# Performance work log

Hardware: AMD Instinct MI355X
Metric: run time of the kernel (lower is better)

## Reference

```python
import jax, jax.numpy as jnp
import numpy as np

E, D, H, T = 8, 1024, 4096, 32768  # experts, model dim, ffn hidden dim, total tokens


def setup_inputs() -> dict:
    key = jax.random.key(0)
    kx, k1, k2, k3 = jax.random.split(key, 4)
    x = jax.random.normal(kx, (T, D), dtype=jnp.float32)
    w1 = jax.random.normal(k1, (E, D, H), dtype=jnp.float32)
    w2 = jax.random.normal(k2, (E, H, D), dtype=jnp.float32)
    w3 = jax.random.normal(k3, (E, D, H), dtype=jnp.float32)
    # uniform token-to-expert split, matching the source's splits = [T//E]*E
    splits = jnp.full((E,), T // E, dtype=jnp.int32)
    return {"x": x, "w1": w1, "w2": w2, "w3": w3, "splits": splits}


def reference(x, w1, w2, w3, splits):
    # splits is uniform (T//E per expert), so torch.split + per-expert matmul +
    # concat is exactly a batched (grouped) GEMM over the expert axis.
    E, D, H = w1.shape
    xe = x.reshape(E, -1, D)  # [E, T//E, D]
    gate = jnp.einsum('etd,edh->eth', xe, w1)  # w1 projection
    up = jnp.einsum('etd,edh->eth', xe, w3)    # w3 projection
    h = jax.nn.silu(gate) * up                 # fused SwiGLU activation
    out = jnp.einsum('eth,ehd->etd', h, w2)    # down projection
    return out.reshape(x.shape)
```

## Files before the change

kernel.cpp:

```cpp
#include <hip/hip_runtime.h>
#include <stdint.h>

#define E_  8
#define D_  1024
#define H_  4096
#define T_  32768
#define TPE 4096

typedef __bf16 bf16x8 __attribute__((ext_vector_type(8)));
typedef float  f32x4  __attribute__((ext_vector_type(4)));
typedef unsigned short u16x4 __attribute__((ext_vector_type(4)));
typedef unsigned short u16x8 __attribute__((ext_vector_type(8)));

__device__ __forceinline__ unsigned short f2bf(float f) {
  union { float f; uint32_t u; } v; v.f = f;
  uint32_t u = v.u;
  return (unsigned short)((u + 0x7FFFu + ((u >> 16) & 1u)) >> 16);
}

__device__ __forceinline__ void gld16(const unsigned short* g, unsigned short* l) {
  __builtin_amdgcn_global_load_lds(
      (const __attribute__((address_space(1))) unsigned int*)g,
      (__attribute__((address_space(3))) unsigned int*)l, 16, 0, 0);
}

__device__ __forceinline__ f32x4 mfma_bf16(bf16x8 a, bf16x8 b, f32x4 c) {
  return __builtin_amdgcn_mfma_f32_16x16x32_bf16(a, b, c, 0, 0, 0);
}

__global__ void cvt_bf16(const float* __restrict__ in, unsigned short* __restrict__ out) {
  size_t i = ((size_t)blockIdx.x * 256 + threadIdx.x) * 8;
  float4 a = *(const float4*)(in + i);
  float4 b = *(const float4*)(in + i + 4);
  u16x8 o;
  o[0] = f2bf(a.x); o[1] = f2bf(a.y); o[2] = f2bf(a.z); o[3] = f2bf(a.w);
  o[4] = f2bf(b.x); o[5] = f2bf(b.y); o[6] = f2bf(b.z); o[7] = f2bf(b.w);
  *(u16x8*)(out + i) = o;
}

__global__ void transpose_bf16(const float* __restrict__ in, unsigned short* __restrict__ out,
                               int R, int C) {
  __shared__ unsigned short t[64][68];
  size_t eo = (size_t)blockIdx.z * R * C;
  const float* ine = in + eo;
  unsigned short* oute = out + eo;
  int r0 = blockIdx.y * 64, c0 = blockIdx.x * 64;
  int rl = threadIdx.x >> 4;
  int cl = (threadIdx.x & 15) * 4;
#pragma unroll
  for (int i = 0; i < 4; ++i) {
    int r = i * 16 + rl;
    float4 v = *(const float4*)(ine + (size_t)(r0 + r) * C + c0 + cl);
    t[cl + 0][r] = f2bf(v.x);
    t[cl + 1][r] = f2bf(v.y);
    t[cl + 2][r] = f2bf(v.z);
    t[cl + 3][r] = f2bf(v.w);
  }
  __syncthreads();
#pragma unroll
  for (int i = 0; i < 4; ++i) {
    int c = i * 16 + rl;
    *(u16x4*)(oute + (size_t)(c0 + c) * R + r0 + cl) = *(const u16x4*)&t[c][cl];
  }
}

__global__ void transpose_ilv_bf16(const float* __restrict__ in, unsigned short* __restrict__ out,
                                   int R, int C, int off) {
  __shared__ unsigned short t[64][68];
  const float* ine = in + (size_t)blockIdx.z * R * C;
  unsigned short* oute = out + (size_t)blockIdx.z * 2 * (size_t)R * C;
  int r0 = blockIdx.y * 64, c0 = blockIdx.x * 64;
  int rl = threadIdx.x >> 4;
  int cl = (threadIdx.x & 15) * 4;
#pragma unroll
  for (int i = 0; i < 4; ++i) {
    int r = i * 16 + rl;
    float4 v = *(const float4*)(ine + (size_t)(r0 + r) * C + c0 + cl);
    t[cl + 0][r] = f2bf(v.x);
    t[cl + 1][r] = f2bf(v.y);
    t[cl + 2][r] = f2bf(v.z);
    t[cl + 3][r] = f2bf(v.w);
  }
  __syncthreads();
#pragma unroll
  for (int i = 0; i < 4; ++i) {
    int c = i * 16 + rl;
    int rr = c0 + c;
    int orow = 32 * (rr >> 4) + (rr & 15) + off;
    *(u16x4*)(oute + (size_t)orow * R + r0 + cl) = *(const u16x4*)&t[c][cl];
  }
}

template<int KT>
__device__ __forceinline__ void gemm_core(
    const unsigned short* __restrict__ A,
    const unsigned short* __restrict__ B,
    const int K, const int m0, const int n0,
    unsigned short* sm, f32x4 (&acc)[8][4]) {
  const int tid  = threadIdx.x;
  const int w    = tid >> 6;
  const int lane = tid & 63;
  const int wr = w >> 2, wc = w & 3;
  const int lr = lane & 15, lk = lane >> 4;

  const unsigned short* gA[4];
  const unsigned short* gB[4];
#pragma unroll
  for (int q = 0; q < 4; ++q) {
    const int rg = 4 * q + (w >> 1);
    const size_t ro = (size_t)(rg * 16 + lr) * K + (w & 1) * 32 + lk * 8;
    gA[q] = A + (size_t)m0 * K + ro;
    gB[q] = B + (size_t)n0 * K + ro;
  }

#pragma unroll
  for (int q = 0; q < 4; ++q) gld16(gA[q], sm + (w + 8 * q) * 512);
#pragma unroll
  for (int q = 0; q < 4; ++q) gld16(gB[q], sm + 32768 + (w + 8 * q) * 512);
  gld16(gB[0] + 64, sm + 32768 + 16384 + (w + 0) * 512);
  gld16(gB[1] + 64, sm + 32768 + 16384 + (w + 8) * 512);
  gld16(gA[0] + 64, sm + 16384 + (w + 0) * 512);
  gld16(gA[1] + 64, sm + 16384 + (w + 8) * 512);
  asm volatile("s_waitcnt vmcnt(4)" ::: "memory");
  __builtin_amdgcn_s_barrier();

  bf16x8 a[4][2], bb[4][2];

#pragma unroll 1
  for (int u = 0; u < KT; ++u) {
    const int bu = u & 1;
    unsigned short* cA = sm + bu * 16384;
    unsigned short* cB = sm + 32768 + bu * 16384;
    unsigned short* nA = sm + (bu ^ 1) * 16384;
    unsigned short* nB = sm + 32768 + (bu ^ 1) * 16384;
    const int koff1 = (u + 1) * 64, koff2 = (u + 2) * 64;

#pragma unroll
    for (int i = 0; i < 4; ++i)
#pragma unroll
      for (int kc = 0; kc < 2; ++kc)
        a[i][kc] = *(const bf16x8*)(cA + ((wr * 8 + i) * 2 + kc) * 512 + lane * 8);
#pragma unroll
    for (int j = 0; j < 2; ++j)
#pragma unroll
      for (int kc = 0; kc < 2; ++kc)
        bb[j][kc] = *(const bf16x8*)(cB + ((wc * 4 + j) * 2 + kc) * 512 + lane * 8);
    if (u + 1 < KT) {
      gld16(gA[2] + koff1, nA + (w + 16) * 512);
      gld16(gA[3] + koff1, nA + (w + 24) * 512);
    }
    __builtin_amdgcn_s_barrier();
    asm volatile("s_waitcnt lgkmcnt(0)" ::: "memory");
    __builtin_amdgcn_sched_barrier(0);
    __builtin_amdgcn_s_setprio(1);
#pragma unroll
    for (int i = 0; i < 4; ++i)
#pragma unroll
      for (int j = 0; j < 2; ++j)
#pragma unroll
        for (int kc = 0; kc < 2; ++kc)
          acc[i][j] = mfma_bf16(a[i][kc], bb[j][kc], acc[i][j]);
    __builtin_amdgcn_s_setprio(0);
    __builtin_amdgcn_s_barrier();

#pragma unroll
    for (int j = 0; j < 2; ++j)
#pragma unroll
      for (int kc = 0; kc < 2; ++kc)
        bb[2 + j][kc] = *(const bf16x8*)(cB + ((wc * 4 + 2 + j) * 2 + kc) * 512 + lane * 8);
    if (u + 1 < KT) {
      gld16(gB[2] + koff1, nB + (w + 16) * 512);
      gld16(gB[3] + koff1, nB + (w + 24) * 512);
    }
    __builtin_amdgcn_s_barrier();
    asm volatile("s_waitcnt lgkmcnt(0)" ::: "memory");
    __builtin_amdgcn_sched_barrier(0);
    __builtin_amdgcn_s_setprio(1);
#pragma unroll
    for (int i = 0; i < 4; ++i)
#pragma unroll
      for (int j = 0; j < 2; ++j)
#pragma unroll
        for (int kc = 0; kc < 2; ++kc)
          acc[i][2 + j] = mfma_bf16(a[i][kc], bb[2 + j][kc], acc[i][2 + j]);
    __builtin_amdgcn_s_setprio(0);
    __builtin_amdgcn_s_barrier();

#pragma unroll
    for (int i = 0; i < 4; ++i)
#pragma unroll
      for (int kc = 0; kc < 2; ++kc)
        a[i][kc] = *(const bf16x8*)(cA + ((wr * 8 + 4 + i) * 2 + kc) * 512 + lane * 8);
    if (u + 2 < KT) {
      gld16(gB[0] + koff2, cB + (w + 0) * 512);
      gld16(gB[1] + koff2, cB + (w + 8) * 512);
    }
    __builtin_amdgcn_s_barrier();
    asm volatile("s_waitcnt lgkmcnt(0)" ::: "memory");
    __builtin_amdgcn_sched_barrier(0);
    __builtin_amdgcn_s_setprio(1);
#pragma unroll
    for (int i = 0; i < 4; ++i)
#pragma unroll
      for (int j = 0; j < 2; ++j)
#pragma unroll
        for (int kc = 0; kc < 2; ++kc)
          acc[4 + i][j] = mfma_bf16(a[i][kc], bb[j][kc], acc[4 + i][j]);
    __builtin_amdgcn_s_setprio(0);
    __builtin_amdgcn_s_barrier();

    if (u + 2 < KT) {
      gld16(gA[0] + koff2, cA + (w + 0) * 512);
      gld16(gA[1] + koff2, cA + (w + 8) * 512);
    }
    __builtin_amdgcn_s_barrier();
    __builtin_amdgcn_s_setprio(1);
#pragma unroll
    for (int i = 0; i < 4; ++i)
#pragma unroll
      for (int j = 0; j < 2; ++j)
#pragma unroll
        for (int kc = 0; kc < 2; ++kc)
          acc[4 + i][2 + j] = mfma_bf16(a[i][kc], bb[2 + j][kc], acc[4 + i][2 + j]);
    __builtin_amdgcn_s_setprio(0);
    if (u == KT - 2) {
      asm volatile("s_waitcnt vmcnt(0)" ::: "memory");
    } else {
      asm volatile("s_waitcnt vmcnt(4)" ::: "memory");
    }
    __builtin_amdgcn_s_barrier();
  }
}

__global__ __launch_bounds__(512, 2) void gemm_gateup(
    const unsigned short* __restrict__ xb,
    const unsigned short* __restrict__ w13t,
    unsigned short* __restrict__ hbuf) {
  __shared__ __align__(16) unsigned short sm[65536];
  const int e = blockIdx.z;
  const int bid = blockIdx.x;
  const int sb = (bid & 7) * 64 + (bid >> 3);
  const int mb = sb & 15, nb = sb >> 4;
  const int m0 = mb * 256, n0 = nb * 256;

  f32x4 acc[8][4] = {};
  gemm_core<D_ / 64>(xb + (size_t)e * TPE * D_,
                     w13t + (size_t)e * (2 * H_) * D_,
                     D_, m0, n0, sm, acc);

  const int tid = threadIdx.x;
  const int w = tid >> 6, lane = tid & 63;
  const int wr = w >> 2, wc = w & 3, lr = lane & 15, lk = lane >> 4;
  unsigned short* He = hbuf + (size_t)e * TPE * H_;
  const int rbase = m0 + wr * 128;
  const int cbase = n0 / 2 + wc * 32;
#pragma unroll
  for (int i = 0; i < 8; ++i)
#pragma unroll
    for (int jp = 0; jp < 2; ++jp)
#pragma unroll
      for (int r = 0; r < 4; ++r) {
        float g  = acc[i][2 * jp][r];
        float uu = acc[i][2 * jp + 1][r];
        float hv = (g / (1.0f + __expf(-g))) * uu;
        He[(size_t)(rbase + i * 16 + lk * 4 + r) * H_ + cbase + jp * 16 + lr] = f2bf(hv);
      }
}

__global__ __launch_bounds__(512, 2) void gemm_down(
    const unsigned short* __restrict__ hbuf,
    const unsigned short* __restrict__ w2t,
    float* __restrict__ out) {
  __shared__ __align__(16) unsigned short sm[65536];
  const int e = blockIdx.z;
  const int bid = blockIdx.x;
  const int sb = (bid & 7) * 8 + (bid >> 3);
  const int mb = sb & 15, nb = sb >> 4;
  const int m0 = mb * 256, n0 = nb * 256;

  f32x4 acc[8][4] = {};
  gemm_core<H_ / 64>(hbuf + (size_t)e * TPE * H_,
                     w2t + (size_t)e * (size_t)D_ * H_,
                     H_, m0, n0, sm, acc);

  const int tid = threadIdx.x;
  const int w = tid >> 6, lane = tid & 63;
  const int wr = w >> 2, wc = w & 3, lr = lane & 15, lk = lane >> 4;
  float* Oe = out + (size_t)e * TPE * D_;
  const int rbase = m0 + wr * 128;
  const int cbase = n0 + wc * 64;
#pragma unroll
  for (int i = 0; i < 8; ++i)
#pragma unroll
    for (int j = 0; j < 4; ++j)
#pragma unroll
      for (int r = 0; r < 4; ++r)
        Oe[(size_t)(rbase + i * 16 + lk * 4 + r) * D_ + cbase + j * 16 + lr] = acc[i][j][r];
}

extern "C" void kernel_launch(void* const* d_in, const int* in_sizes, int n_in,
                              void* d_out, int out_size, void* d_ws, size_t ws_size,
                              hipStream_t stream) {
  const float* x  = (const float*)d_in[0];
  const float* w1 = (const float*)d_in[1];
  const float* w2 = (const float*)d_in[2];
  const float* w3 = (const float*)d_in[3];

  char* ws = (char*)d_ws;
  unsigned short* xb   = (unsigned short*)(ws);
  unsigned short* w13t = (unsigned short*)(ws + (64ull << 20));
  unsigned short* w2t  = (unsigned short*)(ws + (192ull << 20));
  unsigned short* hbuf = (unsigned short*)(ws + (256ull << 20));
  float* out = (float*)d_out;

  cvt_bf16<<<(T_ * D_) / 2048, 256, 0, stream>>>(x, xb);
  transpose_ilv_bf16<<<dim3(H_ / 64, D_ / 64, E_), 256, 0, stream>>>(w1, w13t, D_, H_, 0);
  transpose_ilv_bf16<<<dim3(H_ / 64, D_ / 64, E_), 256, 0, stream>>>(w3, w13t, D_, H_, 16);
  transpose_bf16<<<dim3(D_ / 64, H_ / 64, E_), 256, 0, stream>>>(w2, w2t, H_, D_);

  gemm_gateup<<<dim3(512, 1, E_), 512, 0, stream>>>(xb, w13t, hbuf);

  gemm_down<<<dim3(64, 1, E_), 512, 0, stream>>>(hbuf, w2t, out);
}
```

Before: 1.360 ms.

## Switch GEMM core from 16x16x32 to 32x32x16 bf16 MFMA tiles

Replaces the 16x16x32 MFMA instruction with the 32x32x16 variant in the shared GEMM core. This changes the LDS fragment layout, the global-to-LDS load addressing, the w1/w3 interleave granularity (32-row groups) and both epilogues to match the 32x32 accumulator layout. Larger MFMA tiles mean fewer instructions and fewer LDS reads per FLOP. The trade-off is a different register pressure profile and epilogue store pattern.

```diff
diff --git a/kernel.cpp b/kernel.cpp
--- a/kernel.cpp
+++ b/kernel.cpp
@@ -9,6 +9,7 @@
 
 typedef __bf16 bf16x8 __attribute__((ext_vector_type(8)));
 typedef float  f32x4  __attribute__((ext_vector_type(4)));
+typedef float  f32x16 __attribute__((ext_vector_type(16)));
 typedef unsigned short u16x4 __attribute__((ext_vector_type(4)));
 typedef unsigned short u16x8 __attribute__((ext_vector_type(8)));
 
@@ -24,8 +25,8 @@
       (__attribute__((address_space(3))) unsigned int*)l, 16, 0, 0);
 }
 
-__device__ __forceinline__ f32x4 mfma_bf16(bf16x8 a, bf16x8 b, f32x4 c) {
-  return __builtin_amdgcn_mfma_f32_16x16x32_bf16(a, b, c, 0, 0, 0);
+__device__ __forceinline__ f32x16 mfma32(bf16x8 a, bf16x8 b, f32x16 c) {
+  return __builtin_amdgcn_mfma_f32_32x32x16_bf16(a, b, c, 0, 0, 0);
 }
 
 __global__ void cvt_bf16(const float* __restrict__ in, unsigned short* __restrict__ out) {
@@ -86,7 +87,7 @@
   for (int i = 0; i < 4; ++i) {
     int c = i * 16 + rl;
     int rr = c0 + c;
-    int orow = 32 * (rr >> 4) + (rr & 15) + off;
+    int orow = 64 * (rr >> 5) + (rr & 31) + off;
     *(u16x4*)(oute + (size_t)orow * R + r0 + cl) = *(const u16x4*)&t[c][cl];
   }
 }
@@ -96,19 +97,21 @@
     const unsigned short* __restrict__ A,
     const unsigned short* __restrict__ B,
     const int K, const int m0, const int n0,
-    unsigned short* sm, f32x4 (&acc)[8][4]) {
+    unsigned short* sm, f32x16 (&acc)[4][2]) {
   const int tid  = threadIdx.x;
   const int w    = tid >> 6;
   const int lane = tid & 63;
   const int wr = w >> 2, wc = w & 3;
-  const int lr = lane & 15, lk = lane >> 4;
+  const int lr = lane & 31;
+  const int lh = lane >> 5;
 
   const unsigned short* gA[4];
   const unsigned short* gB[4];
 #pragma unroll
   for (int q = 0; q < 4; ++q) {
-    const int rg = 4 * q + (w >> 1);
-    const size_t ro = (size_t)(rg * 16 + lr) * K + (w & 1) * 32 + lk * 8;
+    const int c  = w + 8 * q;
+    const int rb = c >> 2, kc = c & 3;
+    const size_t ro = (size_t)(rb * 32 + lr) * K + kc * 16 + lh * 8;
     gA[q] = A + (size_t)m0 * K + ro;
     gB[q] = B + (size_t)n0 * K + ro;
   }
@@ -124,7 +127,7 @@
   asm volatile("s_waitcnt vmcnt(4)" ::: "memory");
   __builtin_amdgcn_s_barrier();
 
-  bf16x8 a[4][2], bb[4][2];
+  bf16x8 a[2][4], bb[2][4];
 
 #pragma unroll 1
   for (int u = 0; u < KT; ++u) {
@@ -136,15 +139,13 @@
     const int koff1 = (u + 1) * 64, koff2 = (u + 2) * 64;
 
 #pragma unroll
-    for (int i = 0; i < 4; ++i)
-#pragma unroll
-      for (int kc = 0; kc < 2; ++kc)
-        a[i][kc] = *(const bf16x8*)(cA + ((wr * 8 + i) * 2 + kc) * 512 + lane * 8);
-#pragma unroll
-    for (int j = 0; j < 2; ++j)
-#pragma unroll
-      for (int kc = 0; kc < 2; ++kc)
-        bb[j][kc] = *(const bf16x8*)(cB + ((wc * 4 + j) * 2 + kc) * 512 + lane * 8);
+    for (int i = 0; i < 2; ++i)
+#pragma unroll
+      for (int ks = 0; ks < 4; ++ks)
+        a[i][ks] = *(const bf16x8*)(cA + ((wr * 4 + i) * 4 + ks) * 512 + lane * 8);
+#pragma unroll
+    for (int ks = 0; ks < 4; ++ks)
+      bb[0][ks] = *(const bf16x8*)(cB + ((wc * 2 + 0) * 4 + ks) * 512 + lane * 8);
     if (u + 1 < KT) {
       gld16(gA[2] + koff1, nA + (w + 16) * 512);
       gld16(gA[3] + koff1, nA + (w + 24) * 512);
@@ -154,20 +155,16 @@
     __builtin_amdgcn_sched_barrier(0);
     __builtin_amdgcn_s_setprio(1);
 #pragma unroll
-    for (int i = 0; i < 4; ++i)
-#pragma unroll
-      for (int j = 0; j < 2; ++j)
-#pragma unroll
-        for (int kc = 0; kc < 2; ++kc)
-          acc[i][j] = mfma_bf16(a[i][kc], bb[j][kc], acc[i][j]);
+    for (int ks = 0; ks < 4; ++ks)
+#pragma unroll
+      for (int i = 0; i < 2; ++i)
+        acc[i][0] = mfma32(a[i][ks], bb[0][ks], acc[i][0]);
     __builtin_amdgcn_s_setprio(0);
     __builtin_amdgcn_s_barrier();
 
 #pragma unroll
-    for (int j = 0; j < 2; ++j)
-#pragma unroll
-      for (int kc = 0; kc < 2; ++kc)
-        bb[2 + j][kc] = *(const bf16x8*)(cB + ((wc * 4 + 2 + j) * 2 + kc) * 512 + lane * 8);
+    for (int ks = 0; ks < 4; ++ks)
+      bb[1][ks] = *(const bf16x8*)(cB + ((wc * 2 + 1) * 4 + ks) * 512 + lane * 8);
     if (u + 1 < KT) {
       gld16(gB[2] + koff1, nB + (w + 16) * 512);
       gld16(gB[3] + koff1, nB + (w + 24) * 512);
@@ -177,20 +174,18 @@
     __builtin_amdgcn_sched_barrier(0);
     __builtin_amdgcn_s_setprio(1);
 #pragma unroll
-    for (int i = 0; i < 4; ++i)
-#pragma unroll
-      for (int j = 0; j < 2; ++j)
-#pragma unroll
-        for (int kc = 0; kc < 2; ++kc)
-          acc[i][2 + j] = mfma_bf16(a[i][kc], bb[2 + j][kc], acc[i][2 + j]);
+    for (int ks = 0; ks < 4; ++ks)
+#pragma unroll
+      for (int i = 0; i < 2; ++i)
+        acc[i][1] = mfma32(a[i][ks], bb[1][ks], acc[i][1]);
     __builtin_amdgcn_s_setprio(0);
     __builtin_amdgcn_s_barrier();
 
 #pragma unroll
-    for (int i = 0; i < 4; ++i)
-#pragma unroll
-      for (int kc = 0; kc < 2; ++kc)
-        a[i][kc] = *(const bf16x8*)(cA + ((wr * 8 + 4 + i) * 2 + kc) * 512 + lane * 8);
+    for (int i = 0; i < 2; ++i)
+#pragma unroll
+      for (int ks = 0; ks < 4; ++ks)
+        a[i][ks] = *(const bf16x8*)(cA + ((wr * 4 + 2 + i) * 4 + ks) * 512 + lane * 8);
     if (u + 2 < KT) {
       gld16(gB[0] + koff2, cB + (w + 0) * 512);
       gld16(gB[1] + koff2, cB + (w + 8) * 512);
@@ -200,12 +195,10 @@
     __builtin_amdgcn_sched_barrier(0);
     __builtin_amdgcn_s_setprio(1);
 #pragma unroll
-    for (int i = 0; i < 4; ++i)
-#pragma unroll
-      for (int j = 0; j < 2; ++j)
-#pragma unroll
-        for (int kc = 0; kc < 2; ++kc)
-          acc[4 + i][j] = mfma_bf16(a[i][kc], bb[j][kc], acc[4 + i][j]);
+    for (int ks = 0; ks < 4; ++ks)
+#pragma unroll
+      for (int i = 0; i < 2; ++i)
+        acc[2 + i][0] = mfma32(a[i][ks], bb[0][ks], acc[2 + i][0]);
     __builtin_amdgcn_s_setprio(0);
     __builtin_amdgcn_s_barrier();
 
@@ -216,12 +209,10 @@
     __builtin_amdgcn_s_barrier();
     __builtin_amdgcn_s_setprio(1);
 #pragma unroll
-    for (int i = 0; i < 4; ++i)
-#pragma unroll
-      for (int j = 0; j < 2; ++j)
-#pragma unroll
-        for (int kc = 0; kc < 2; ++kc)
-          acc[4 + i][2 + j] = mfma_bf16(a[i][kc], bb[2 + j][kc], acc[4 + i][2 + j]);
+    for (int ks = 0; ks < 4; ++ks)
+#pragma unroll
+      for (int i = 0; i < 2; ++i)
+        acc[2 + i][1] = mfma32(a[i][ks], bb[1][ks], acc[2 + i][1]);
     __builtin_amdgcn_s_setprio(0);
     if (u == KT - 2) {
       asm volatile("s_waitcnt vmcnt(0)" ::: "memory");
@@ -243,28 +234,27 @@
   const int mb = sb & 15, nb = sb >> 4;
   const int m0 = mb * 256, n0 = nb * 256;
 
-  f32x4 acc[8][4] = {};
+  f32x16 acc[4][2] = {};
   gemm_core<D_ / 64>(xb + (size_t)e * TPE * D_,
                      w13t + (size_t)e * (2 * H_) * D_,
                      D_, m0, n0, sm, acc);
 
   const int tid = threadIdx.x;
   const int w = tid >> 6, lane = tid & 63;
-  const int wr = w >> 2, wc = w & 3, lr = lane & 15, lk = lane >> 4;
+  const int wr = w >> 2, wc = w & 3;
   unsigned short* He = hbuf + (size_t)e * TPE * H_;
-  const int rbase = m0 + wr * 128;
-  const int cbase = n0 / 2 + wc * 32;
-#pragma unroll
-  for (int i = 0; i < 8; ++i)
-#pragma unroll
-    for (int jp = 0; jp < 2; ++jp)
-#pragma unroll
-      for (int r = 0; r < 4; ++r) {
-        float g  = acc[i][2 * jp][r];
-        float uu = acc[i][2 * jp + 1][r];
-        float hv = (g / (1.0f + __expf(-g))) * uu;
-        He[(size_t)(rbase + i * 16 + lk * 4 + r) * H_ + cbase + jp * 16 + lr] = f2bf(hv);
-      }
+  const int rbase = m0 + wr * 128 + 4 * (lane >> 5);
+  const int hcol  = n0 / 2 + wc * 32 + (lane & 31);
+#pragma unroll
+  for (int mi = 0; mi < 4; ++mi)
+#pragma unroll
+    for (int r = 0; r < 16; ++r) {
+      float g  = acc[mi][0][r];
+      float uu = acc[mi][1][r];
+      float hv = (g / (1.0f + __expf(-g))) * uu;
+      int row = rbase + mi * 32 + (r & 3) + 8 * (r >> 2);
+      He[(size_t)row * H_ + hcol] = f2bf(hv);
+    }
 }
 
 __global__ __launch_bounds__(512, 2) void gemm_down(
@@ -278,24 +268,26 @@
   const int mb = sb & 15, nb = sb >> 4;
   const int m0 = mb * 256, n0 = nb * 256;
 
-  f32x4 acc[8][4] = {};
+  f32x16 acc[4][2] = {};
   gemm_core<H_ / 64>(hbuf + (size_t)e * TPE * H_,
                      w2t + (size_t)e * (size_t)D_ * H_,
                      H_, m0, n0, sm, acc);
 
   const int tid = threadIdx.x;
   const int w = tid >> 6, lane = tid & 63;
-  const int wr = w >> 2, wc = w & 3, lr = lane & 15, lk = lane >> 4;
+  const int wr = w >> 2, wc = w & 3;
   float* Oe = out + (size_t)e * TPE * D_;
-  const int rbase = m0 + wr * 128;
-  const int cbase = n0 + wc * 64;
-#pragma unroll
-  for (int i = 0; i < 8; ++i)
-#pragma unroll
-    for (int j = 0; j < 4; ++j)
-#pragma unroll
-      for (int r = 0; r < 4; ++r)
-        Oe[(size_t)(rbase + i * 16 + lk * 4 + r) * D_ + cbase + j * 16 + lr] = acc[i][j][r];
+  const int rbase = m0 + wr * 128 + 4 * (lane >> 5);
+  const int cbase = n0 + wc * 64 + (lane & 31);
+#pragma unroll
+  for (int mi = 0; mi < 4; ++mi)
+#pragma unroll
+    for (int nj = 0; nj < 2; ++nj)
+#pragma unroll
+      for (int r = 0; r < 16; ++r) {
+        int row = rbase + mi * 32 + (r & 3) + 8 * (r >> 2);
+        Oe[(size_t)row * D_ + cbase + nj * 32] = acc[mi][nj][r];
+      }
 }
 
 extern "C" void kernel_launch(void* const* d_in, const int* in_sizes, int n_in,
@@ -315,7 +307,7 @@
 
   cvt_bf16<<<(T_ * D_) / 2048, 256, 0, stream>>>(x, xb);
   transpose_ilv_bf16<<<dim3(H_ / 64, D_ / 64, E_), 256, 0, stream>>>(w1, w13t, D_, H_, 0);
-  transpose_ilv_bf16<<<dim3(H_ / 64, D_ / 64, E_), 256, 0, stream>>>(w3, w13t, D_, H_, 16);
+  transpose_ilv_bf16<<<dim3(H_ / 64, D_ / 64, E_), 256, 0, stream>>>(w3, w13t, D_, H_, 32);
   transpose_bf16<<<dim3(D_ / 64, H_ / 64, E_), 256, 0, stream>>>(w2, w2t, H_, D_);
 
   gemm_gateup<<<dim3(512, 1, E_), 512, 0, stream>>>(xb, w13t, hbuf);
```

Measured after the change: 1.424 ms. +4.7%, slower.

## Make GEMM blocks persistent over M tiles with a continuous k-pipeline

Applied to the files above, without the earlier changes.

Both the gate/up and down GEMMs now launch one block per N tile (and per M pair for down). Each block iterates over several 256-row M tiles with a single flattened load/MFMA pipeline, running the epilogue and zeroing accumulators at each tile boundary. The aim is to remove per-tile prologue and drain costs and keep global-to-LDS prefetch running across tiles. The trade-off is that the grid shrinks to 256 blocks, which fills only one of the two block slots per CU that the launch bounds allow. Epilogue stores also now stall the pipeline instead of overlapping with another resident block.

```diff
diff --git a/kernel.cpp b/kernel.cpp
--- a/kernel.cpp
+++ b/kernel.cpp
@@ -91,49 +91,61 @@
   }
 }
 
-template<int KT>
-__device__ __forceinline__ void gemm_core(
+template<int KT, int NT, typename EPI>
+__device__ __forceinline__ void gemm_persist(
     const unsigned short* __restrict__ A,
     const unsigned short* __restrict__ B,
-    const int K, const int m0, const int n0,
-    unsigned short* sm, f32x4 (&acc)[8][4]) {
+    const int K, unsigned short* sm, f32x4 (&acc)[8][4], EPI epi) {
+  constexpr int V = KT * NT;
+  constexpr int LOGKT = (KT == 16) ? 4 : 6;
+  static_assert(KT == (1 << LOGKT), "KT must be 16 or 64");
   const int tid  = threadIdx.x;
   const int w    = tid >> 6;
   const int lane = tid & 63;
   const int wr = w >> 2, wc = w & 3;
   const int lr = lane & 15, lk = lane >> 4;
 
+  auto aoff = [&](int vv) -> size_t {
+    return (size_t)((vv >> LOGKT) * 256) * (size_t)K + (size_t)((vv & (KT - 1)) * 64);
+  };
+  auto boff = [&](int vv) -> size_t {
+    return (size_t)((vv & (KT - 1)) * 64);
+  };
+
   const unsigned short* gA[4];
   const unsigned short* gB[4];
 #pragma unroll
   for (int q = 0; q < 4; ++q) {
     const int rg = 4 * q + (w >> 1);
     const size_t ro = (size_t)(rg * 16 + lr) * K + (w & 1) * 32 + lk * 8;
-    gA[q] = A + (size_t)m0 * K + ro;
-    gB[q] = B + (size_t)n0 * K + ro;
-  }
-
-#pragma unroll
-  for (int q = 0; q < 4; ++q) gld16(gA[q], sm + (w + 8 * q) * 512);
-#pragma unroll
-  for (int q = 0; q < 4; ++q) gld16(gB[q], sm + 32768 + (w + 8 * q) * 512);
-  gld16(gB[0] + 64, sm + 32768 + 16384 + (w + 0) * 512);
-  gld16(gB[1] + 64, sm + 32768 + 16384 + (w + 8) * 512);
-  gld16(gA[0] + 64, sm + 16384 + (w + 0) * 512);
-  gld16(gA[1] + 64, sm + 16384 + (w + 8) * 512);
+    gA[q] = A + ro;
+    gB[q] = B + ro;
+  }
+
+  {
+    const size_t a1 = aoff(1), b1 = boff(1);
+#pragma unroll
+    for (int q = 0; q < 4; ++q) gld16(gA[q], sm + (w + 8 * q) * 512);
+#pragma unroll
+    for (int q = 0; q < 4; ++q) gld16(gB[q], sm + 32768 + (w + 8 * q) * 512);
+    gld16(gB[0] + b1, sm + 32768 + 16384 + (w + 0) * 512);
+    gld16(gB[1] + b1, sm + 32768 + 16384 + (w + 8) * 512);
+    gld16(gA[0] + a1, sm + 16384 + (w + 0) * 512);
+    gld16(gA[1] + a1, sm + 16384 + (w + 8) * 512);
+  }
   asm volatile("s_waitcnt vmcnt(4)" ::: "memory");
   __builtin_amdgcn_s_barrier();
 
   bf16x8 a[4][2], bb[4][2];
 
 #pragma unroll 1
-  for (int u = 0; u < KT; ++u) {
-    const int bu = u & 1;
+  for (int v = 0; v < V; ++v) {
+    const int bu = v & 1;
     unsigned short* cA = sm + bu * 16384;
     unsigned short* cB = sm + 32768 + bu * 16384;
     unsigned short* nA = sm + (bu ^ 1) * 16384;
     unsigned short* nB = sm + 32768 + (bu ^ 1) * 16384;
-    const int koff1 = (u + 1) * 64, koff2 = (u + 2) * 64;
+    const int v1 = v + 1, v2 = v + 2;
 
 #pragma unroll
     for (int i = 0; i < 4; ++i)
@@ -145,9 +157,10 @@
 #pragma unroll
       for (int kc = 0; kc < 2; ++kc)
         bb[j][kc] = *(const bf16x8*)(cB + ((wc * 4 + j) * 2 + kc) * 512 + lane * 8);
-    if (u + 1 < KT) {
-      gld16(gA[2] + koff1, nA + (w + 16) * 512);
-      gld16(gA[3] + koff1, nA + (w + 24) * 512);
+    if (v1 < V) {
+      const size_t ao = aoff(v1);
+      gld16(gA[2] + ao, nA + (w + 16) * 512);
+      gld16(gA[3] + ao, nA + (w + 24) * 512);
     }
     __builtin_amdgcn_s_barrier();
     asm volatile("s_waitcnt lgkmcnt(0)" ::: "memory");
@@ -168,9 +181,10 @@
 #pragma unroll
       for (int kc = 0; kc < 2; ++kc)
         bb[2 + j][kc] = *(const bf16x8*)(cB + ((wc * 4 + 2 + j) * 2 + kc) * 512 + lane * 8);
-    if (u + 1 < KT) {
-      gld16(gB[2] + koff1, nB + (w + 16) * 512);
-      gld16(gB[3] + koff1, nB + (w + 24) * 512);
+    if (v1 < V) {
+      const size_t bo = boff(v1);
+      gld16(gB[2] + bo, nB + (w + 16) * 512);
+      gld16(gB[3] + bo, nB + (w + 24) * 512);
     }
     __builtin_amdgcn_s_barrier();
     asm volatile("s_waitcnt lgkmcnt(0)" ::: "memory");
@@ -191,9 +205,10 @@
 #pragma unroll
       for (int kc = 0; kc < 2; ++kc)
         a[i][kc] = *(const bf16x8*)(cA + ((wr * 8 + 4 + i) * 2 + kc) * 512 + lane * 8);
-    if (u + 2 < KT) {
-      gld16(gB[0] + koff2, cB + (w + 0) * 512);
-      gld16(gB[1] + koff2, cB + (w + 8) * 512);
+    if (v2 < V) {
+      const size_t bo = boff(v2);
+      gld16(gB[0] + bo, cB + (w + 0) * 512);
+      gld16(gB[1] + bo, cB + (w + 8) * 512);
     }
     __builtin_amdgcn_s_barrier();
     asm volatile("s_waitcnt lgkmcnt(0)" ::: "memory");
@@ -209,9 +224,10 @@
     __builtin_amdgcn_s_setprio(0);
     __builtin_amdgcn_s_barrier();
 
-    if (u + 2 < KT) {
-      gld16(gA[0] + koff2, cA + (w + 0) * 512);
-      gld16(gA[1] + koff2, cA + (w + 8) * 512);
+    if (v2 < V) {
+      const size_t ao = aoff(v2);
+      gld16(gA[0] + ao, cA + (w + 0) * 512);
+      gld16(gA[1] + ao, cA + (w + 8) * 512);
     }
     __builtin_amdgcn_s_barrier();
     __builtin_amdgcn_s_setprio(1);
@@ -223,12 +239,21 @@
         for (int kc = 0; kc < 2; ++kc)
           acc[4 + i][2 + j] = mfma_bf16(a[i][kc], bb[2 + j][kc], acc[4 + i][2 + j]);
     __builtin_amdgcn_s_setprio(0);
-    if (u == KT - 2) {
+    if (v == V - 2) {
       asm volatile("s_waitcnt vmcnt(0)" ::: "memory");
     } else {
       asm volatile("s_waitcnt vmcnt(4)" ::: "memory");
     }
     __builtin_amdgcn_s_barrier();
+
+    if ((v & (KT - 1)) == (KT - 1)) {
+      epi(v >> LOGKT);
+#pragma unroll
+      for (int i = 0; i < 8; ++i)
+#pragma unroll
+        for (int j = 0; j < 4; ++j)
+          acc[i][j] = f32x4{0.f, 0.f, 0.f, 0.f};
+    }
   }
 }
 
@@ -237,34 +262,35 @@
     const unsigned short* __restrict__ w13t,
     unsigned short* __restrict__ hbuf) {
   __shared__ __align__(16) unsigned short sm[65536];
-  const int e = blockIdx.z;
-  const int bid = blockIdx.x;
-  const int sb = (bid & 7) * 64 + (bid >> 3);
-  const int mb = sb & 15, nb = sb >> 4;
-  const int m0 = mb * 256, n0 = nb * 256;
-
-  f32x4 acc[8][4] = {};
-  gemm_core<D_ / 64>(xb + (size_t)e * TPE * D_,
-                     w13t + (size_t)e * (2 * H_) * D_,
-                     D_, m0, n0, sm, acc);
+  const int e  = blockIdx.z;
+  const int nb = blockIdx.x;
+  const int n0 = nb * 256;
+
+  const unsigned short* A = xb + (size_t)e * TPE * D_;
+  const unsigned short* B = w13t + (size_t)e * (2 * H_) * D_ + (size_t)n0 * D_;
+  unsigned short* He = hbuf + (size_t)e * TPE * H_;
 
   const int tid = threadIdx.x;
   const int w = tid >> 6, lane = tid & 63;
   const int wr = w >> 2, wc = w & 3, lr = lane & 15, lk = lane >> 4;
-  unsigned short* He = hbuf + (size_t)e * TPE * H_;
-  const int rbase = m0 + wr * 128;
-  const int cbase = n0 / 2 + wc * 32;
-#pragma unroll
-  for (int i = 0; i < 8; ++i)
-#pragma unroll
-    for (int jp = 0; jp < 2; ++jp)
-#pragma unroll
-      for (int r = 0; r < 4; ++r) {
-        float g  = acc[i][2 * jp][r];
-        float uu = acc[i][2 * jp + 1][r];
-        float hv = (g / (1.0f + __expf(-g))) * uu;
-        He[(size_t)(rbase + i * 16 + lk * 4 + r) * H_ + cbase + jp * 16 + lr] = f2bf(hv);
-      }
+
+  f32x4 acc[8][4] = {};
+  auto epi = [&](int t) {
+    const int rbase = t * 256 + wr * 128;
+    const int cbase = n0 / 2 + wc * 32;
+#pragma unroll
+    for (int i = 0; i < 8; ++i)
+#pragma unroll
+      for (int jp = 0; jp < 2; ++jp)
+#pragma unroll
+        for (int r = 0; r < 4; ++r) {
+          float g  = acc[i][2 * jp][r];
+          float uu = acc[i][2 * jp + 1][r];
+          float hv = (g / (1.0f + __expf(-g))) * uu;
+          He[(size_t)(rbase + i * 16 + lk * 4 + r) * H_ + cbase + jp * 16 + lr] = f2bf(hv);
+        }
+  };
+  gemm_persist<16, 16>(A, B, D_, sm, acc, epi);
 }
 
 __global__ __launch_bounds__(512, 2) void gemm_down(
@@ -272,30 +298,33 @@
     const unsigned short* __restrict__ w2t,
     float* __restrict__ out) {
   __shared__ __align__(16) unsigned short sm[65536];
-  const int e = blockIdx.z;
-  const int bid = blockIdx.x;
-  const int sb = (bid & 7) * 8 + (bid >> 3);
-  const int mb = sb & 15, nb = sb >> 4;
-  const int m0 = mb * 256, n0 = nb * 256;
-
-  f32x4 acc[8][4] = {};
-  gemm_core<H_ / 64>(hbuf + (size_t)e * TPE * H_,
-                     w2t + (size_t)e * (size_t)D_ * H_,
-                     H_, m0, n0, sm, acc);
+  const int e  = blockIdx.z;
+  const int x  = blockIdx.x;
+  const int nb = x & 3, mp = x >> 2;
+  const int n0 = nb * 256;
+  const int mbase = mp * 512;
+
+  const unsigned short* A = hbuf + (size_t)e * TPE * H_ + (size_t)mbase * H_;
+  const unsigned short* B = w2t + (size_t)e * (size_t)D_ * H_ + (size_t)n0 * H_;
+  float* Oe = out + (size_t)e * TPE * D_;
 
   const int tid = threadIdx.x;
   const int w = tid >> 6, lane = tid & 63;
   const int wr = w >> 2, wc = w & 3, lr = lane & 15, lk = lane >> 4;
-  float* Oe = out + (size_t)e * TPE * D_;
-  const int rbase = m0 + wr * 128;
-  const int cbase = n0 + wc * 64;
-#pragma unroll
-  for (int i = 0; i < 8; ++i)
-#pragma unroll
-    for (int j = 0; j < 4; ++j)
-#pragma unroll
-      for (int r = 0; r < 4; ++r)
-        Oe[(size_t)(rbase + i * 16 + lk * 4 + r) * D_ + cbase + j * 16 + lr] = acc[i][j][r];
+
+  f32x4 acc[8][4] = {};
+  auto epi = [&](int t) {
+    const int rbase = mbase + t * 256 + wr * 128;
+    const int cbase = n0 + wc * 64;
+#pragma unroll
+    for (int i = 0; i < 8; ++i)
+#pragma unroll
+      for (int j = 0; j < 4; ++j)
+#pragma unroll
+        for (int r = 0; r < 4; ++r)
+          Oe[(size_t)(rbase + i * 16 + lk * 4 + r) * D_ + cbase + j * 16 + lr] = acc[i][j][r];
+  };
+  gemm_persist<64, 2>(A, B, H_, sm, acc, epi);
 }
 
 extern "C" void kernel_launch(void* const* d_in, const int* in_sizes, int n_in,
@@ -318,7 +347,7 @@
   transpose_ilv_bf16<<<dim3(H_ / 64, D_ / 64, E_), 256, 0, stream>>>(w3, w13t, D_, H_, 16);
   transpose_bf16<<<dim3(D_ / 64, H_ / 64, E_), 256, 0, stream>>>(w2, w2t, H_, D_);
 
-  gemm_gateup<<<dim3(512, 1, E_), 512, 0, stream>>>(xb, w13t, hbuf);
-
-  gemm_down<<<dim3(64, 1, E_), 512, 0, stream>>>(hbuf, w2t, out);
-}
+  gemm_gateup<<<dim3(32, 1, E_), 512, 0, stream>>>(xb, w13t, hbuf);
+
+  gemm_down<<<dim3(32, 1, E_), 512, 0, stream>>>(hbuf, w2t, out);
+}
```

New measurement: 1.333 ms. -2.0%, faster.
